# Performance work log

Hardware: AMD Instinct MI355X
Metric: run time of the kernel (lower is better)

The kernel has to match this reference:

```python
import jax, jax.numpy as jnp
import numpy as np

H, DH = 4, 64          # heads, dim_head (match init_kwargs)
E = 128                # edge_dim
INNER = H * DH
NEG = -jnp.finfo(jnp.float32).max


def setup_inputs() -> dict:
    key = jax.random.key(0)
    ks = jax.random.split(key, 8)
    b, i, j = 1, 256, 256
    s = lambda fan_in: 1.0 / np.sqrt(fan_in)
    return {
        "inter_edges": jax.random.normal(ks[0], (b, i, j, E), jnp.float32),
        "ab_mask": jnp.ones((b, i), dtype=bool),
        "at_mask": jnp.ones((b, j), dtype=bool),
        "Wq": jax.random.normal(ks[1], (E, INNER), jnp.float32) * s(E),
        "Wk": jax.random.normal(ks[2], (E, INNER), jnp.float32) * s(E),
        "Wv": jax.random.normal(ks[3], (E, INNER), jnp.float32) * s(E),
        "Web": jax.random.normal(ks[4], (E, H), jnp.float32) * s(E),
        "Wg": jax.random.normal(ks[5], (E, INNER), jnp.float32) * s(E),
        "bg": jnp.zeros((INNER,), jnp.float32),
        "Wo": jax.random.normal(ks[6], (INNER, E), jnp.float32) * s(INNER),
        "bo": jnp.zeros((E,), jnp.float32),
    }


def reference(inter_edges, ab_mask, at_mask, Wq, Wk, Wv, Web, Wg, bg, Wo, bo):
    b, i, j, e = inter_edges.shape  # b must be 1 (bias broadcast in original)

    def split_hd(t):  # 'b i j (h d) -> (b h) i j d'
        return t.reshape(b, i, j, H, DH).transpose(0, 3, 1, 2, 4).reshape(b * H, i, j, DH)

    q = split_hd(inter_edges @ Wq)
    k = split_hd(inter_edges @ Wk)
    v = split_hd(inter_edges @ Wv)

    # to_ebias: [b,i,j,h].transpose(0,-1) -> [h,i,j,b]; broadcasts over key axis (b==1)
    z_bias = jnp.swapaxes(inter_edges @ Web, 0, -1)

    # gate uses (d h) split order, unlike q/k/v's (h d)
    gate = jax.nn.sigmoid(inter_edges @ Wg + bg)
    z_gate = gate.reshape(b, i, j, DH, H).transpose(0, 4, 1, 2, 3).reshape(b * H, i, j, DH)

    sim = jnp.einsum('hijd,hikd->hijk', q, k) * (DH ** -0.5) + z_bias

    mask = ab_mask[:, :, None] & at_mask[:, None, :]          # [b,i,j]
    mask = jnp.repeat(mask, H, axis=0)                        # [(b h),i,j]
    sim = jnp.where(mask[..., None], sim, NEG)                # mask whole (i,j) query rows

    attn = jax.nn.softmax(sim, axis=-1)
    # original einsum 'h i j k, h i j d -> h i j d' == v * attn.sum(-1)
    out = v * jnp.sum(attn, axis=-1, keepdims=True)
    out = z_gate * out
    out = out.reshape(b, H, i, j, DH).transpose(0, 2, 3, 1, 4).reshape(b, i, j, INNER)
    return out @ Wo + bo
```

## Files before the change

kernel.cpp:

```cpp
#include <hip/hip_runtime.h>
#include <hip/hip_bf16.h>

typedef __attribute__((ext_vector_type(8))) short short8;
typedef __attribute__((ext_vector_type(4))) float f32x4;

__device__ __forceinline__ unsigned short f2b(float x) {
  union { float f; unsigned u; } v; v.f = x;
  unsigned r = v.u + 0x7fffu + ((v.u >> 16) & 1u);
  return (unsigned short)(r >> 16);
}

__device__ __forceinline__ ushort4 pack4(float4 f) {
  union { __hip_bfloat162 h[2]; ushort4 s; } u;
  u.h[0] = __float22bfloat162_rn(float2{f.x, f.y});
  u.h[1] = __float22bfloat162_rn(float2{f.z, f.w});
  return u.s;
}

__global__ __launch_bounds__(256) void prep_kernel(
    const float* __restrict__ Wv, const float* __restrict__ Wg,
    const float* __restrict__ bgv, const float* __restrict__ Wo,
    unsigned short* __restrict__ W1T, unsigned short* __restrict__ WoT,
    float* __restrict__ bg2)
{
  int t = blockIdx.x * 256 + threadIdx.x;
  if (t < 32768) {
    int e = t >> 8, c = t & 255;
    W1T[c * 128 + e] = f2b(Wv[t]);
  } else if (t < 65536) {
    int s = t - 32768;
    int e = s >> 8, g = s & 255;
    int cc = ((g & 3) << 6) + (g >> 2);
    W1T[(256 + cc) * 128 + e] = f2b(Wg[s]);
  } else if (t < 65536 + 32768) {
    int s = t - 65536;
    int c = s >> 7, o = s & 127;
    WoT[o * 256 + c] = f2b(Wo[s]);
  } else if (t < 65536 + 32768 + 256) {
    int g = t - (65536 + 32768);
    bg2[((g & 3) << 6) + (g >> 2)] = bgv[g];
  }
}

__global__ __launch_bounds__(512) void fused_kernel(
    const float* __restrict__ X,
    const unsigned short* __restrict__ W1T,
    const unsigned short* __restrict__ WoT,
    const float* __restrict__ bg2,
    const float* __restrict__ bo,
    float* __restrict__ Out)
{
  __shared__ unsigned short Xs[2][32 * 128];
  __shared__ unsigned short Ys[2][32 * 256];

  const int tid  = threadIdx.x;
  const int lane = tid & 63;
  const int wave = tid >> 6;
  const int l15  = lane & 15;
  const int lhi  = lane >> 4;
  const long rowbase0 = (long)blockIdx.x * 256;

  short8 wS1[2][4][2];
  float  bgt[2];
  #pragma unroll
  for (int t = 0; t < 2; ++t) {
    int c0 = (wave * 2 + t) * 16;
    const unsigned short* base = W1T + (c0 + l15) * 128 + lhi * 8;
    #pragma unroll
    for (int ks = 0; ks < 4; ++ks) {
      wS1[t][ks][0] = *reinterpret_cast<const short8*>(base + ks * 32);
      wS1[t][ks][1] = *reinterpret_cast<const short8*>(base + ks * 32 + 256 * 128);
    }
    bgt[t] = bg2[c0 + l15];
  }
  short8 wS2[8];
  const int o0 = wave * 16;
  #pragma unroll
  for (int ks = 0; ks < 8; ++ks)
    wS2[ks] = *reinterpret_cast<const short8*>(WoT + (o0 + l15) * 256 + ks * 32 + lhi * 8);
  const float bov = bo[o0 + l15];

  const int r0 = tid >> 5,        c0v = (tid & 31) * 4;
  const int s0w = (r0 * 128 + c0v) ^ ((r0 & 7) << 3);
  const int r1 = (512 + tid) >> 5;
  const int s1w = (r1 * 128 + c0v) ^ ((r1 & 7) << 3);

  {
    const float4* Xp = reinterpret_cast<const float4*>(X + rowbase0 * 128);
    float4 a = Xp[tid], b = Xp[512 + tid];
    *reinterpret_cast<ushort4*>(&Xs[0][s0w]) = pack4(a);
    *reinterpret_cast<ushort4*>(&Xs[0][s1w]) = pack4(b);
  }
  float4 pf0, pf1;
  {
    const float4* Xp = reinterpret_cast<const float4*>(X + (rowbase0 + 32) * 128);
    pf0 = Xp[tid]; pf1 = Xp[512 + tid];
  }
  __syncthreads();

  const f32x4 vzero = {0.f, 0.f, 0.f, 0.f};

  #pragma unroll
  for (int i = 0; i < 8; ++i) {
    const int cb = i & 1;

    short8 afrag[2][4];
    #pragma unroll
    for (int mt = 0; mt < 2; ++mt) {
      int row = mt * 16 + l15;
      #pragma unroll
      for (int ks = 0; ks < 4; ++ks) {
        int sidx = (row * 128 + ks * 32 + lhi * 8) ^ ((row & 7) << 3);
        afrag[mt][ks] = *reinterpret_cast<const short8*>(&Xs[cb][sidx]);
      }
    }

    __builtin_amdgcn_s_setprio(1);
    f32x4 accV[2][2], accG[2][2];
    #pragma unroll
    for (int t = 0; t < 2; ++t) {
      #pragma unroll
      for (int mt = 0; mt < 2; ++mt) { accV[t][mt] = vzero; accG[t][mt] = vzero; }
      #pragma unroll
      for (int ks = 0; ks < 4; ++ks) {
        #pragma unroll
        for (int mt = 0; mt < 2; ++mt) {
          accV[t][mt] = __builtin_amdgcn_mfma_f32_16x16x32_bf16(afrag[mt][ks], wS1[t][ks][0], accV[t][mt], 0, 0, 0);
          accG[t][mt] = __builtin_amdgcn_mfma_f32_16x16x32_bf16(afrag[mt][ks], wS1[t][ks][1], accG[t][mt], 0, 0, 0);
        }
      }
    }
    __builtin_amdgcn_s_setprio(0);
    #pragma unroll
    for (int t = 0; t < 2; ++t) {
      int c0 = (wave * 2 + t) * 16;
      #pragma unroll
      for (int mt = 0; mt < 2; ++mt) {
        #pragma unroll
        for (int r = 0; r < 4; ++r) {
          int row = mt * 16 + lhi * 4 + r;
          float z = accG[t][mt][r] + bgt[t];
          float g = 1.0f / (1.0f + __expf(-z));
          float y = g * accV[t][mt][r];
          int sidx = (row * 256 + c0 + l15) ^ ((row & 7) << 3);
          Ys[cb][sidx] = f2b(y);
        }
      }
    }

    if (i < 7) {
      float4 a = pf0, b = pf1;
      *reinterpret_cast<ushort4*>(&Xs[cb ^ 1][s0w]) = pack4(a);
      *reinterpret_cast<ushort4*>(&Xs[cb ^ 1][s1w]) = pack4(b);
      if (i < 6) {
        const float4* Xp = reinterpret_cast<const float4*>(X + (rowbase0 + (long)(i + 2) * 32) * 128);
        pf0 = Xp[tid]; pf1 = Xp[512 + tid];
      }
    }

    __syncthreads();

    f32x4 acc2[2] = {vzero, vzero};
    #pragma unroll
    for (int ks = 0; ks < 8; ++ks) {
      #pragma unroll
      for (int mt = 0; mt < 2; ++mt) {
        int row = mt * 16 + l15;
        int sidx = (row * 256 + ks * 32 + lhi * 8) ^ ((row & 7) << 3);
        short8 a = *reinterpret_cast<const short8*>(&Ys[cb][sidx]);
        acc2[mt] = __builtin_amdgcn_mfma_f32_16x16x32_bf16(a, wS2[ks], acc2[mt], 0, 0, 0);
      }
    }
    const long rowb = rowbase0 + (long)i * 32;
    #pragma unroll
    for (int mt = 0; mt < 2; ++mt) {
      #pragma unroll
      for (int r = 0; r < 4; ++r) {
        Out[(rowb + mt * 16 + lhi * 4 + r) * 128 + o0 + l15] = acc2[mt][r] + bov;
      }
    }
  }
}

extern "C" void kernel_launch(void* const* d_in, const int* in_sizes, int n_in,
                              void* d_out, int out_size, void* d_ws, size_t ws_size,
                              hipStream_t stream) {
  const float* X   = (const float*)d_in[0];
  const float* Wv  = (const float*)d_in[5];
  const float* Wg  = (const float*)d_in[7];
  const float* bg  = (const float*)d_in[8];
  const float* Wo  = (const float*)d_in[9];
  const float* bo  = (const float*)d_in[10];

  unsigned short* W1T = (unsigned short*)d_ws;
  unsigned short* WoT = W1T + 512 * 128;
  float*          bg2 = (float*)(WoT + 128 * 256);

  prep_kernel<<<386, 256, 0, stream>>>(Wv, Wg, bg, Wo, W1T, WoT, bg2);

  float* Out = (float*)d_out;
  fused_kernel<<<256, 512, 0, stream>>>(X, W1T, WoT, bg2, bo, Out);
}
```

Baseline: 117.3 us.

## Software-pipeline output GEMM of previous tile with gate GEMM of next tile

Splits the loop body into stage1 (input tile to gated bf16 activations) and stage2 (output projection). Each barrier interval now holds stage2 of tile i together with stage1 of tile i+1, and the global prefetch of X runs one tile further ahead. The aim is to hide global load latency and barrier stalls behind MFMA work from two different tiles. It also switches the sigmoid to a hardware reciprocal and uses packed bf16 conversion. The cost is higher register pressure from keeping more work live at once, and a slightly less exact sigmoid.

New measurement: 115.9 us. Within noise of the previous version (-1.2%).

```diff
diff --git a/kernel.cpp b/kernel.cpp
--- a/kernel.cpp
+++ b/kernel.cpp
@@ -85,25 +85,20 @@
   const int r1 = (512 + tid) >> 5;
   const int s1w = (r1 * 128 + c0v) ^ ((r1 & 7) << 3);
 
-  {
-    const float4* Xp = reinterpret_cast<const float4*>(X + rowbase0 * 128);
-    float4 a = Xp[tid], b = Xp[512 + tid];
-    *reinterpret_cast<ushort4*>(&Xs[0][s0w]) = pack4(a);
-    *reinterpret_cast<ushort4*>(&Xs[0][s1w]) = pack4(b);
-  }
   float4 pf0, pf1;
-  {
-    const float4* Xp = reinterpret_cast<const float4*>(X + (rowbase0 + 32) * 128);
+  const f32x4 vzero = {0.f, 0.f, 0.f, 0.f};
+
+  auto issuePf = [&](int k) {
+    const float4* Xp = reinterpret_cast<const float4*>(X + (rowbase0 + (long)k * 32) * 128);
     pf0 = Xp[tid]; pf1 = Xp[512 + tid];
-  }
-  __syncthreads();
-
-  const f32x4 vzero = {0.f, 0.f, 0.f, 0.f};
-
-  #pragma unroll
-  for (int i = 0; i < 8; ++i) {
-    const int cb = i & 1;
-
+  };
+  auto drainPf = [&](int k) {
+    *reinterpret_cast<ushort4*>(&Xs[k & 1][s0w]) = pack4(pf0);
+    *reinterpret_cast<ushort4*>(&Xs[k & 1][s1w]) = pack4(pf1);
+  };
+
+  auto stage1 = [&](int k) {
+    const int cb = k & 1;
     short8 afrag[2][4];
     #pragma unroll
     for (int mt = 0; mt < 2; ++mt) {
@@ -114,7 +109,6 @@
         afrag[mt][ks] = *reinterpret_cast<const short8*>(&Xs[cb][sidx]);
       }
     }
-
     __builtin_amdgcn_s_setprio(1);
     f32x4 accV[2][2], accG[2][2];
     #pragma unroll
@@ -136,30 +130,28 @@
       int c0 = (wave * 2 + t) * 16;
       #pragma unroll
       for (int mt = 0; mt < 2; ++mt) {
+        float ys[4];
         #pragma unroll
         for (int r = 0; r < 4; ++r) {
-          int row = mt * 16 + lhi * 4 + r;
           float z = accG[t][mt][r] + bgt[t];
-          float g = 1.0f / (1.0f + __expf(-z));
-          float y = g * accV[t][mt][r];
-          int sidx = (row * 256 + c0 + l15) ^ ((row & 7) << 3);
-          Ys[cb][sidx] = f2b(y);
+          float e = __expf(-z);
+          ys[r] = accV[t][mt][r] * __builtin_amdgcn_rcpf(1.0f + e);
         }
-      }
-    }
-
-    if (i < 7) {
-      float4 a = pf0, b = pf1;
-      *reinterpret_cast<ushort4*>(&Xs[cb ^ 1][s0w]) = pack4(a);
-      *reinterpret_cast<ushort4*>(&Xs[cb ^ 1][s1w]) = pack4(b);
-      if (i < 6) {
-        const float4* Xp = reinterpret_cast<const float4*>(X + (rowbase0 + (long)(i + 2) * 32) * 128);
-        pf0 = Xp[tid]; pf1 = Xp[512 + tid];
-      }
-    }
-
-    __syncthreads();
-
+        __hip_bfloat162 p01 = __float22bfloat162_rn(float2{ys[0], ys[1]});
+        __hip_bfloat162 p23 = __float22bfloat162_rn(float2{ys[2], ys[3]});
+        ushort2 u01 = *reinterpret_cast<ushort2*>(&p01);
+        ushort2 u23 = *reinterpret_cast<ushort2*>(&p23);
+        int rb = mt * 16 + lhi * 4;
+        Ys[cb][((rb + 0) * 256 + c0 + l15) ^ (((rb + 0) & 7) << 3)] = u01.x;
+        Ys[cb][((rb + 1) * 256 + c0 + l15) ^ (((rb + 1) & 7) << 3)] = u01.y;
+        Ys[cb][((rb + 2) * 256 + c0 + l15) ^ (((rb + 2) & 7) << 3)] = u23.x;
+        Ys[cb][((rb + 3) * 256 + c0 + l15) ^ (((rb + 3) & 7) << 3)] = u23.y;
+      }
+    }
+  };
+
+  auto stage2 = [&](int k) {
+    const int cb = k & 1;
     f32x4 acc2[2] = {vzero, vzero};
     #pragma unroll
     for (int ks = 0; ks < 8; ++ks) {
@@ -171,7 +163,7 @@
         acc2[mt] = __builtin_amdgcn_mfma_f32_16x16x32_bf16(a, wS2[ks], acc2[mt], 0, 0, 0);
       }
     }
-    const long rowb = rowbase0 + (long)i * 32;
+    const long rowb = rowbase0 + (long)k * 32;
     #pragma unroll
     for (int mt = 0; mt < 2; ++mt) {
       #pragma unroll
@@ -179,7 +171,31 @@
         Out[(rowb + mt * 16 + lhi * 4 + r) * 128 + o0 + l15] = acc2[mt][r] + bov;
       }
     }
-  }
+  };
+
+  {
+    const float4* Xp = reinterpret_cast<const float4*>(X + rowbase0 * 128);
+    float4 a = Xp[tid], b = Xp[512 + tid];
+    *reinterpret_cast<ushort4*>(&Xs[0][s0w]) = pack4(a);
+    *reinterpret_cast<ushort4*>(&Xs[0][s1w]) = pack4(b);
+    issuePf(1);
+  }
+  __syncthreads();
+
+  stage1(0);
+  drainPf(1);
+  issuePf(2);
+  __syncthreads();
+
+  #pragma unroll
+  for (int i = 0; i < 7; ++i) {
+    stage2(i);
+    stage1(i + 1);
+    if (i + 2 <= 7) drainPf(i + 2);
+    if (i + 3 <= 7) issuePf(i + 3);
+    __syncthreads();
+  }
+  stage2(7);
 }
 
 extern "C" void kernel_launch(void* const* d_in, const int* in_sizes, int n_in,
```
